# Kernel tuning notes

Measured on AMD Instinct MI355X. Metric: run time of the kernel, lower is better.

## Reference

```python
import jax, jax.numpy as jnp
import numpy as np

B, S, E, H = 4, 2048, 512, 1024

def setup_inputs() -> dict:
    key = jax.random.key(0)
    ks = jax.random.split(key, 8)
    s = 1.0 / np.sqrt(H)
    return {
        "hidden_states": jax.random.normal(ks[0], (B, S, H), jnp.float32),
        "external_embeddings": jax.random.normal(ks[1], (B, E, H), jnp.float32),
        "Wq": jax.random.normal(ks[2], (H, H), jnp.float32) * s,
        "bq": jax.random.normal(ks[3], (H,), jnp.float32) * 0.02,
        "Wk": jax.random.normal(ks[4], (H, H), jnp.float32) * s,
        "bk": jax.random.normal(ks[5], (H,), jnp.float32) * 0.02,
        "Wv": jax.random.normal(ks[6], (H, H), jnp.float32) * s,
        "bv": jax.random.normal(ks[7], (H,), jnp.float32) * 0.02,
    }

def reference(hidden_states, external_embeddings, Wq, bq, Wk, bk, Wv, bv):
    # Projections (torch Linear semantics: here weights stored as [in,out])
    q = hidden_states @ Wq + bq              # [B,S,H]
    k_tok = hidden_states @ Wk + bk          # [B,S,H]
    v_tok = hidden_states @ Wv + bv          # [B,S,H]
    k_ext = external_embeddings @ Wk + bk    # [B,E,H]
    v_ext = external_embeddings @ Wv + bv    # [B,E,H]
    # Each token attends to [its own key] ++ [external keys]; NO 1/sqrt(d) scaling
    # and NO head splitting, matching the original forward exactly.
    s_self = jnp.einsum('bsh,bsh->bs', q, k_tok)[..., None]   # [B,S,1]
    s_ext = jnp.einsum('bsh,beh->bse', q, k_ext)              # [B,S,E]
    scores = jnp.concatenate([s_self, s_ext], axis=-1)        # [B,S,1+E]
    probs = jax.nn.softmax(scores, axis=-1)
    ctx = probs[..., :1] * v_tok + jnp.einsum('bse,beh->bsh', probs[..., 1:], v_ext)
    return ctx  # [B,S,H]
```

## Files before the change

### kernel.cpp

```cpp
#include <hip/hip_runtime.h>
#include <stdint.h>

#define BB 4
#define SS 2048
#define EE 512
#define HH 1024

typedef _Float16 f16;
typedef __attribute__((ext_vector_type(8))) _Float16 f16x8;
typedef __attribute__((ext_vector_type(4))) _Float16 f16x4;
typedef __attribute__((ext_vector_type(4))) float f32x4;

__device__ __forceinline__ void async16(void* lds, const void* g) {
  __builtin_amdgcn_global_load_lds(
      (const __attribute__((address_space(1))) unsigned int*)g,
      (__attribute__((address_space(3))) unsigned int*)lds, 16, 0, 0);
}

template <int TERMS>
__device__ __forceinline__ void gemm_core(
    const f16* Ah, const f16* Al, const f16* Bh, const f16* Bl, int K, int ld,
    f16* lAh, f16* lAl, f16* lBh, f16* lBl, f32x4 acc[4][4]) {
  const int tid = threadIdx.x;
  const int wave = tid >> 6;
  const int lane = tid & 63;
  const int lrow = lane >> 2;
  const int lcol = (((lane & 3) ^ ((lane >> 3) & 3))) * 8;
  const int waveM = (wave >> 1) * 64;
  const int waveN = (wave & 1) * 64;
  const int frow = lane & 15;
  const int fk = ((lane >> 4) ^ ((frow >> 1) & 3)) * 8;

  for (int k0 = 0; k0 < K; k0 += 32) {
    __syncthreads();
#pragma unroll
    for (int i = 0; i < 2; ++i) {
      const int r0 = (wave * 2 + i) * 16;
      const size_t goff = (size_t)(r0 + lrow) * ld + (k0 + lcol);
      async16(&lAh[r0 * 32], Ah + goff);
      async16(&lBh[r0 * 32], Bh + goff);
      if (TERMS >= 2) async16(&lBl[r0 * 32], Bl + goff);
      if (TERMS >= 3) async16(&lAl[r0 * 32], Al + goff);
    }
    __syncthreads();

    f16x8 a[4], bh[4], bl[4], al[4];
#pragma unroll
    for (int i = 0; i < 4; ++i) {
      a[i] = *(const f16x8*)&lAh[(waveM + i * 16 + frow) * 32 + fk];
      bh[i] = *(const f16x8*)&lBh[(waveN + i * 16 + frow) * 32 + fk];
      if (TERMS >= 2) bl[i] = *(const f16x8*)&lBl[(waveN + i * 16 + frow) * 32 + fk];
      if (TERMS >= 3) al[i] = *(const f16x8*)&lAl[(waveM + i * 16 + frow) * 32 + fk];
    }
#pragma unroll
    for (int i = 0; i < 4; ++i)
#pragma unroll
      for (int j = 0; j < 4; ++j) {
        acc[i][j] = __builtin_amdgcn_mfma_f32_16x16x32_f16(a[i], bh[j], acc[i][j], 0, 0, 0);
        if (TERMS >= 2)
          acc[i][j] = __builtin_amdgcn_mfma_f32_16x16x32_f16(a[i], bl[j], acc[i][j], 0, 0, 0);
        if (TERMS >= 3)
          acc[i][j] = __builtin_amdgcn_mfma_f32_16x16x32_f16(al[i], bh[j], acc[i][j], 0, 0, 0);
      }
  }
}

__device__ __forceinline__ void epi_transposed(
    f16* __restrict__ dst, const f32x4 acc[4][4], const float bias[4], f16* tl) {
  const int tid = threadIdx.x, wave = tid >> 6, lane = tid & 63;
  const int waveM = (wave >> 1) * 64;
  const int colIn16 = lane & 15, quad = lane >> 4;
#pragma unroll
  for (int p = 0; p < 2; ++p) {
    __syncthreads();
    if ((wave & 1) == p) {
#pragma unroll
      for (int i = 0; i < 4; ++i)
#pragma unroll
        for (int j = 0; j < 4; ++j)
#pragma unroll
          for (int r = 0; r < 4; ++r) {
            const int row = waveM + i * 16 + quad * 4 + r;
            const int colL = j * 16 + colIn16;
            tl[colL * 136 + row] = (f16)(acc[i][j][r] + bias[j]);
          }
    }
    __syncthreads();
    for (int c = tid; c < 1024; c += 256) {
      const int colL = c >> 4, ch = c & 15;
      const f16x8 v = *(const f16x8*)&tl[colL * 136 + ch * 8];
      *(f16x8*)&dst[(size_t)(p * 64 + colL) * EE + ch * 8] = v;
    }
  }
}

__global__ __launch_bounds__(256) void cast_kernel(const float* __restrict__ xh32,
                                                   const float* __restrict__ xe32,
                                                   f16* __restrict__ xh,
                                                   f16* __restrict__ xe) {
  const int i = blockIdx.x * 256 + threadIdx.x;
  const int n4h = 8192 * HH / 4;
  const float* src = i < n4h ? xh32 : xe32;
  f16* dst = i < n4h ? xh : xe;
  const int k = i < n4h ? i : i - n4h;
  const float4 v = ((const float4*)src)[k];
  f16x4 o;
  o.x = (f16)v.x; o.y = (f16)v.y; o.z = (f16)v.z; o.w = (f16)v.w;
  ((f16x4*)dst)[k] = o;
}

__global__ void wsplit_kernel(const float* __restrict__ Wq, const float* __restrict__ Wk,
                              const float* __restrict__ Wv, f16* __restrict__ wt_hi,
                              f16* __restrict__ wt_lo) {
  __shared__ float tile[32][33];
  const int k0 = blockIdx.x * 32;
  const int n0g = blockIdx.y * 32;
  const int which = n0g >> 10;
  const float* W = which == 0 ? Wq : (which == 1 ? Wk : Wv);
  const int n0 = n0g & 1023;
  const int tx = threadIdx.x, ty = threadIdx.y;
#pragma unroll
  for (int i = 0; i < 32; i += 8)
    tile[ty + i][tx] = W[(size_t)(k0 + ty + i) * 1024 + n0 + tx];
  __syncthreads();
#pragma unroll
  for (int i = 0; i < 32; i += 8) {
    const int np = n0g + ty + i;
    const float v = tile[tx][ty + i];
    const size_t idx = (size_t)np * 1024 + k0 + tx;
    const f16 h = (f16)v;
    wt_hi[idx] = h;
    wt_lo[idx] = (f16)(v - (float)h);
  }
}

__global__ __launch_bounds__(256, 4) void proj_kernel(
    const f16* __restrict__ xh, const f16* __restrict__ xe,
    const f16* __restrict__ wt_hi, const f16* __restrict__ wt_lo,
    const float* __restrict__ bq, const float* __restrict__ bk,
    const float* __restrict__ bv, f16* __restrict__ q_hi, f16* __restrict__ q_lo,
    f16* __restrict__ kt, f16* __restrict__ vt,
    f16* __restrict__ ke_hi, f16* __restrict__ ke_lo, f16* __restrict__ veT) {
  const int g = blockIdx.x;
  const int j = g & 7;
  const int s = g >> 3;
  int mtile, ntile;
  if (s < 192) {
    const int w = s / 16, r = s % 16;
    ntile = w * 2 + (r & 1);
    mtile = (r >> 1) * 8 + j;
  } else {
    const int s2 = s - 192;
    const int w = s2 >> 2, r = s2 & 3;
    ntile = 8 + w * 2 + (r & 1);
    mtile = 64 + (r >> 1) * 8 + j;
  }
  const bool extRows = (mtile >= 64);

  __shared__ f16 lds[3 * 4096];

  const f16* A = extRows ? xe : xh;
  const int rowA = (extRows ? (mtile - 64) : mtile) * 128;
  const int rowB = ntile * 128;
  const bool split = (ntile < 8) || (extRows && ntile < 16);

  f32x4 acc[4][4];
#pragma unroll
  for (int i = 0; i < 4; ++i)
#pragma unroll
    for (int jj = 0; jj < 4; ++jj)
#pragma unroll
      for (int r = 0; r < 4; ++r) acc[i][jj][r] = 0.0f;

  if (split)
    gemm_core<2>(A + (size_t)rowA * HH, nullptr, wt_hi + (size_t)rowB * HH,
                 wt_lo + (size_t)rowB * HH, HH, HH,
                 lds, nullptr, lds + 4096, lds + 8192, acc);
  else
    gemm_core<1>(A + (size_t)rowA * HH, nullptr, wt_hi + (size_t)rowB * HH,
                 nullptr, HH, HH, lds, nullptr, lds + 4096, nullptr, acc);

  const int tid = threadIdx.x, wave = tid >> 6, lane = tid & 63;
  const int waveM = (wave >> 1) * 64, waveN = (wave & 1) * 64;
  const int colIn16 = lane & 15, rowQuad = (lane >> 4) * 4;
  float bias[4];
#pragma unroll
  for (int jj = 0; jj < 4; ++jj) {
    const int c = ntile * 128 + waveN + jj * 16 + colIn16;
    bias[jj] = c < 1024 ? bq[c] : (c < 2048 ? bk[c - 1024] : bv[c - 2048]);
  }

  if (extRows && ntile >= 16) {
    const int ge0 = (mtile - 64) * 128;
    const int bb = ge0 >> 9, e0 = ge0 & 511;
    epi_transposed(veT + ((size_t)bb * HH + (ntile - 16) * 128) * EE + e0,
                   acc, bias, lds);
    return;
  }

#pragma unroll
  for (int jj = 0; jj < 4; ++jj) {
    const int c = ntile * 128 + waveN + jj * 16 + colIn16;
#pragma unroll
    for (int i = 0; i < 4; ++i) {
#pragma unroll
      for (int r = 0; r < 4; ++r) {
        const int lrowIdx = waveM + i * 16 + rowQuad + r;
        const float val = acc[i][jj][r] + bias[jj];
        if (c < 1024) {
          const size_t idx = (size_t)(mtile * 128 + lrowIdx) * HH + c;
          const f16 h = (f16)val;
          q_hi[idx] = h;
          q_lo[idx] = (f16)(val - (float)h);
        } else if (c < 2048) {
          const int c2 = c - 1024;
          if (!extRows) {
            kt[(size_t)(mtile * 128 + lrowIdx) * HH + c2] = (f16)val;
          } else {
            const int ge = (mtile - 64) * 128 + lrowIdx;
            const size_t idx = (size_t)ge * HH + c2;
            const f16 h = (f16)val;
            ke_hi[idx] = h;
            ke_lo[idx] = (f16)(val - (float)h);
          }
        } else {
          vt[(size_t)(mtile * 128 + lrowIdx) * HH + (c - 2048)] = (f16)val;
        }
      }
    }
  }
}

__global__ __launch_bounds__(256, 4) void score_kernel(
    const f16* __restrict__ q_hi, const f16* __restrict__ q_lo,
    const f16* __restrict__ ke_hi, const f16* __restrict__ ke_lo,
    float* __restrict__ s_part) {
  const int b = blockIdx.z & 3;
  const int khalf = blockIdx.z >> 2;
  const int mtile = blockIdx.y;
  const int ntile = blockIdx.x;
  __shared__ f16 lds[4 * 4096];
  const size_t aoff = ((size_t)b * SS + mtile * 128) * HH + khalf * 512;
  const size_t boff = ((size_t)b * EE + ntile * 128) * HH + khalf * 512;

  f32x4 acc[4][4];
#pragma unroll
  for (int i = 0; i < 4; ++i)
#pragma unroll
    for (int j = 0; j < 4; ++j)
#pragma unroll
      for (int r = 0; r < 4; ++r) acc[i][j][r] = 0.0f;

  gemm_core<3>(q_hi + aoff, q_lo + aoff, ke_hi + boff, ke_lo + boff, 512, HH,
               lds, lds + 4096, lds + 8192, lds + 12288, acc);

  float* dst = s_part + (size_t)khalf * BB * SS * EE;
  const int tid = threadIdx.x, wave = tid >> 6, lane = tid & 63;
  const int waveM = (wave >> 1) * 64, waveN = (wave & 1) * 64;
  const int colIn16 = lane & 15, rowQuad = (lane >> 4) * 4;
#pragma unroll
  for (int j = 0; j < 4; ++j) {
    const int e = ntile * 128 + waveN + j * 16 + colIn16;
#pragma unroll
    for (int i = 0; i < 4; ++i)
#pragma unroll
      for (int r = 0; r < 4; ++r) {
        const int s = mtile * 128 + waveM + i * 16 + rowQuad + r;
        dst[((size_t)b * SS + s) * EE + e] = acc[i][j][r];
      }
  }
}

__global__ __launch_bounds__(256) void softmax_kernel(
    const f16* __restrict__ q_hi, const f16* __restrict__ q_lo,
    const f16* __restrict__ kt, const float* __restrict__ s_part,
    f16* __restrict__ probs, float* __restrict__ p_self) {
  const int t = blockIdx.x * 4 + (threadIdx.x >> 6);
  const int lane = threadIdx.x & 63;

  const size_t base = (size_t)t * HH;
  float ss = 0.f;
#pragma unroll
  for (int it = 0; it < 4; ++it) {
    const int off = it * 256 + lane * 4;
    const f16x4 qh = *(const f16x4*)&q_hi[base + off];
    const f16x4 ql = *(const f16x4*)&q_lo[base + off];
    const f16x4 kh = *(const f16x4*)&kt[base + off];
    ss += ((float)qh.x + (float)ql.x) * (float)kh.x;
    ss += ((float)qh.y + (float)ql.y) * (float)kh.y;
    ss += ((float)qh.z + (float)ql.z) * (float)kh.z;
    ss += ((float)qh.w + (float)ql.w) * (float)kh.w;
  }
#pragma unroll
  for (int m = 32; m > 0; m >>= 1) ss += __shfl_xor(ss, m, 64);

  const float* r0 = s_part + (size_t)t * EE;
  const float* r1 = s_part + (size_t)BB * SS * EE + (size_t)t * EE;
  const float4 a0 = *(const float4*)&r0[lane * 4];
  const float4 a1 = *(const float4*)&r0[256 + lane * 4];
  const float4 c0 = *(const float4*)&r1[lane * 4];
  const float4 c1 = *(const float4*)&r1[256 + lane * 4];
  const float v0x = a0.x + c0.x, v0y = a0.y + c0.y, v0z = a0.z + c0.z, v0w = a0.w + c0.w;
  const float v1x = a1.x + c1.x, v1y = a1.y + c1.y, v1z = a1.z + c1.z, v1w = a1.w + c1.w;
  float m = fmaxf(fmaxf(fmaxf(v0x, v0y), fmaxf(v0z, v0w)),
                  fmaxf(fmaxf(v1x, v1y), fmaxf(v1z, v1w)));
#pragma unroll
  for (int sh = 32; sh > 0; sh >>= 1) m = fmaxf(m, __shfl_xor(m, sh, 64));
  m = fmaxf(m, ss);
  const float e0 = __expf(v0x - m), e1 = __expf(v0y - m);
  const float e2 = __expf(v0z - m), e3 = __expf(v0w - m);
  const float e4 = __expf(v1x - m), e5 = __expf(v1y - m);
  const float e6 = __expf(v1z - m), e7 = __expf(v1w - m);
  float sum = ((e0 + e1) + (e2 + e3)) + ((e4 + e5) + (e6 + e7));
#pragma unroll
  for (int sh = 32; sh > 0; sh >>= 1) sum += __shfl_xor(sum, sh, 64);
  const float es = __expf(ss - m);
  const float inv = 1.0f / (sum + es);
  f16x4 p0, p1;
  p0.x = (f16)(e0 * inv); p0.y = (f16)(e1 * inv);
  p0.z = (f16)(e2 * inv); p0.w = (f16)(e3 * inv);
  p1.x = (f16)(e4 * inv); p1.y = (f16)(e5 * inv);
  p1.z = (f16)(e6 * inv); p1.w = (f16)(e7 * inv);
  *(f16x4*)&probs[(size_t)t * EE + lane * 4] = p0;
  *(f16x4*)&probs[(size_t)t * EE + 256 + lane * 4] = p1;
  if (lane == 0) p_self[t] = es * inv;
}

__global__ __launch_bounds__(256, 4) void pv_kernel(
    const f16* __restrict__ probs, const f16* __restrict__ veT,
    const float* __restrict__ p_self, const f16* __restrict__ vt,
    float* __restrict__ out) {
  const int b = blockIdx.z;
  const int mtile = blockIdx.y;
  const int ntile = blockIdx.x;
  __shared__ f16 lds[2 * 4096];
  const size_t aoff = ((size_t)b * SS + mtile * 128) * EE;
  const size_t boff = ((size_t)b * HH + ntile * 128) * EE;

  f32x4 acc[4][4];
#pragma unroll
  for (int i = 0; i < 4; ++i)
#pragma unroll
    for (int j = 0; j < 4; ++j)
#pragma unroll
      for (int r = 0; r < 4; ++r) acc[i][j][r] = 0.0f;

  gemm_core<1>(probs + aoff, nullptr, veT + boff, nullptr, EE, EE,
               lds, nullptr, lds + 4096, nullptr, acc);

  const int tid = threadIdx.x, wave = tid >> 6, lane = tid & 63;
  const int waveM = (wave >> 1) * 64, waveN = (wave & 1) * 64;
  const int colIn16 = lane & 15, rowQuad = (lane >> 4) * 4;
#pragma unroll
  for (int j = 0; j < 4; ++j) {
    const int h = ntile * 128 + waveN + j * 16 + colIn16;
#pragma unroll
    for (int i = 0; i < 4; ++i)
#pragma unroll
      for (int r = 0; r < 4; ++r) {
        const int s = mtile * 128 + waveM + i * 16 + rowQuad + r;
        const size_t t = (size_t)b * SS + s;
        __builtin_nontemporal_store(
            acc[i][j][r] + p_self[t] * (float)vt[t * HH + h], &out[t * HH + h]);
      }
  }
}

extern "C" void kernel_launch(void* const* d_in, const int* in_sizes, int n_in,
                              void* d_out, int out_size, void* d_ws, size_t ws_size,
                              hipStream_t stream) {
  const float* hidden = (const float*)d_in[0];
  const float* ext    = (const float*)d_in[1];
  const float* Wq = (const float*)d_in[2];
  const float* bq = (const float*)d_in[3];
  const float* Wk = (const float*)d_in[4];
  const float* bk = (const float*)d_in[5];
  const float* Wv = (const float*)d_in[6];
  const float* bv = (const float*)d_in[7];
  float* out = (float*)d_out;

  char* ws = (char*)d_ws;
  size_t off = 0;
  auto alloc = [&](size_t bytes) {
    char* p = ws + off;
    off += (bytes + 255) & ~(size_t)255;
    return p;
  };
  const size_t TOK = 8192, EXT = 2048;
  f16* xh    = (f16*)alloc(TOK * HH * 2);
  f16* xe    = (f16*)alloc(EXT * HH * 2);
  f16* wt_hi = (f16*)alloc(3072ull * HH * 2);
  f16* wt_lo = (f16*)alloc(3072ull * HH * 2);
  f16* q_hi  = (f16*)alloc(TOK * HH * 2);
  f16* q_lo  = (f16*)alloc(TOK * HH * 2);
  f16* kt    = (f16*)alloc(TOK * HH * 2);
  f16* vt    = (f16*)alloc(TOK * HH * 2);
  f16* ke_hi = (f16*)alloc(EXT * HH * 2);
  f16* ke_lo = (f16*)alloc(EXT * HH * 2);
  f16* veT   = (f16*)alloc((size_t)BB * HH * EE * 2);
  float* p_self = (float*)alloc(TOK * 4);
  float* s_part = (float*)alloc(2ull * BB * SS * EE * 4);
  f16* probs    = (f16*)alloc((size_t)BB * SS * EE * 2);

  cast_kernel<<<10240, 256, 0, stream>>>(hidden, ext, xh, xe);
  wsplit_kernel<<<dim3(32, 96), dim3(32, 8), 0, stream>>>(Wq, Wk, Wv, wt_hi, wt_lo);

  proj_kernel<<<1792, 256, 0, stream>>>(
      xh, xe, wt_hi, wt_lo, bq, bk, bv,
      q_hi, q_lo, kt, vt, ke_hi, ke_lo, veT);

  score_kernel<<<dim3(4, 16, 8), 256, 0, stream>>>(q_hi, q_lo, ke_hi, ke_lo, s_part);
  softmax_kernel<<<2048, 256, 0, stream>>>(q_hi, q_lo, kt, s_part, probs, p_self);
  pv_kernel<<<dim3(8, 16, 4), 256, 0, stream>>>(probs, veT, p_self, vt, out);
}
```

Before: 332.5 us.

## Use 256-row projection tiles with 512 threads and drop score split-K

The projection GEMM moves to 256x128 tiles run by 512-thread blocks (8 waves), so each weight tile loaded into LDS is reused across twice as many rows. The transposed V-ext epilogue is reworked to match. The score kernel no longer splits K in two, writing one fp32 score buffer instead of two partials, which removes the extra partial write and re-read in softmax. The softmax self-score now drops the q_lo term, using fp16 q_hi only, which trades a little precision for less memory traffic. Fewer, larger blocks and half as many score blocks may lower occupancy and parallelism.

Measured after the change: 349.8 us. 1.05x slower.

```diff
diff --git a/kernel.cpp b/kernel.cpp
--- a/kernel.cpp
+++ b/kernel.cpp
@@ -65,31 +65,82 @@
   }
 }
 
-__device__ __forceinline__ void epi_transposed(
+template <int TERMS>
+__device__ __forceinline__ void gemm_core256(
+    const f16* A, const f16* Bh, const f16* Bl, int K, int ld,
+    f16* lA, f16* lBh, f16* lBl, f32x4 acc[4][4]) {
+  const int tid = threadIdx.x;
+  const int wave = tid >> 6;
+  const int lane = tid & 63;
+  const int lrow = lane >> 2;
+  const int lcol = (((lane & 3) ^ ((lane >> 3) & 3))) * 8;
+  const int waveM = (wave >> 1) * 64;
+  const int waveN = (wave & 1) * 64;
+  const int frow = lane & 15;
+  const int fk = ((lane >> 4) ^ ((frow >> 1) & 3)) * 8;
+
+  for (int k0 = 0; k0 < K; k0 += 32) {
+    __syncthreads();
+    {
+      const int r0 = wave * 16;
+      async16(&lA[r0 * 32], A + (size_t)(r0 + lrow) * ld + (k0 + lcol));
+      const int r1 = 128 + wave * 16;
+      async16(&lA[r1 * 32], A + (size_t)(r1 + lrow) * ld + (k0 + lcol));
+      async16(&lBh[r0 * 32], Bh + (size_t)(r0 + lrow) * ld + (k0 + lcol));
+      if (TERMS >= 2)
+        async16(&lBl[r0 * 32], Bl + (size_t)(r0 + lrow) * ld + (k0 + lcol));
+    }
+    __syncthreads();
+
+    f16x8 a[4], bh[4], bl[4];
+#pragma unroll
+    for (int i = 0; i < 4; ++i) {
+      a[i] = *(const f16x8*)&lA[(waveM + i * 16 + frow) * 32 + fk];
+      bh[i] = *(const f16x8*)&lBh[(waveN + i * 16 + frow) * 32 + fk];
+      if (TERMS >= 2) bl[i] = *(const f16x8*)&lBl[(waveN + i * 16 + frow) * 32 + fk];
+    }
+#pragma unroll
+    for (int i = 0; i < 4; ++i)
+#pragma unroll
+      for (int j = 0; j < 4; ++j) {
+        acc[i][j] = __builtin_amdgcn_mfma_f32_16x16x32_f16(a[i], bh[j], acc[i][j], 0, 0, 0);
+        if (TERMS >= 2)
+          acc[i][j] = __builtin_amdgcn_mfma_f32_16x16x32_f16(a[i], bl[j], acc[i][j], 0, 0, 0);
+      }
+  }
+}
+
+__device__ __forceinline__ void epi_transposed256(
     f16* __restrict__ dst, const f32x4 acc[4][4], const float bias[4], f16* tl) {
   const int tid = threadIdx.x, wave = tid >> 6, lane = tid & 63;
-  const int waveM = (wave >> 1) * 64;
-  const int colIn16 = lane & 15, quad = lane >> 4;
-#pragma unroll
-  for (int p = 0; p < 2; ++p) {
-    __syncthreads();
-    if ((wave & 1) == p) {
-#pragma unroll
-      for (int i = 0; i < 4; ++i)
-#pragma unroll
-        for (int j = 0; j < 4; ++j)
-#pragma unroll
-          for (int r = 0; r < 4; ++r) {
-            const int row = waveM + i * 16 + quad * 4 + r;
-            const int colL = j * 16 + colIn16;
-            tl[colL * 136 + row] = (f16)(acc[i][j][r] + bias[j]);
-          }
-    }
-    __syncthreads();
-    for (int c = tid; c < 1024; c += 256) {
-      const int colL = c >> 4, ch = c & 15;
-      const f16x8 v = *(const f16x8*)&tl[colL * 136 + ch * 8];
-      *(f16x8*)&dst[(size_t)(p * 64 + colL) * EE + ch * 8] = v;
+  const int quad = lane >> 4, colIn16 = lane & 15;
+  const int mq = wave >> 1;
+  const int half = mq >> 1;
+  const int msub = mq & 1;
+  const int np = wave & 1;
+#pragma unroll
+  for (int h = 0; h < 2; ++h) {
+#pragma unroll
+    for (int p = 0; p < 2; ++p) {
+      __syncthreads();
+      if (half == h && np == p) {
+#pragma unroll
+        for (int i = 0; i < 4; ++i)
+#pragma unroll
+          for (int j = 0; j < 4; ++j)
+#pragma unroll
+            for (int r = 0; r < 4; ++r) {
+              const int rowL = msub * 64 + i * 16 + quad * 4 + r;
+              const int colL = j * 16 + colIn16;
+              tl[colL * 136 + rowL] = (f16)(acc[i][j][r] + bias[j]);
+            }
+      }
+      __syncthreads();
+      for (int c = tid; c < 1024; c += 512) {
+        const int colL = c >> 4, ch = c & 15;
+        const f16x8 v = *(const f16x8*)&tl[colL * 136 + ch * 8];
+        *(f16x8*)&dst[(size_t)(p * 64 + colL) * EE + h * 128 + ch * 8] = v;
+      }
     }
   }
 }
@@ -134,7 +185,7 @@
   }
 }
 
-__global__ __launch_bounds__(256, 4) void proj_kernel(
+__global__ __launch_bounds__(512, 4) void proj_kernel(
     const f16* __restrict__ xh, const f16* __restrict__ xe,
     const f16* __restrict__ wt_hi, const f16* __restrict__ wt_lo,
     const float* __restrict__ bq, const float* __restrict__ bk,
@@ -142,25 +193,24 @@
     f16* __restrict__ kt, f16* __restrict__ vt,
     f16* __restrict__ ke_hi, f16* __restrict__ ke_lo, f16* __restrict__ veT) {
   const int g = blockIdx.x;
-  const int j = g & 7;
+  const int xcd = g & 7;
   const int s = g >> 3;
   int mtile, ntile;
-  if (s < 192) {
-    const int w = s / 16, r = s % 16;
+  if (s < 96) {
+    const int w = s >> 3, r = s & 7;
     ntile = w * 2 + (r & 1);
-    mtile = (r >> 1) * 8 + j;
+    mtile = (r >> 1) * 8 + xcd;
   } else {
-    const int s2 = s - 192;
-    const int w = s2 >> 2, r = s2 & 3;
-    ntile = 8 + w * 2 + (r & 1);
-    mtile = 64 + (r >> 1) * 8 + j;
-  }
-  const bool extRows = (mtile >= 64);
-
-  __shared__ f16 lds[3 * 4096];
+    const int s2 = s - 96;
+    ntile = 8 + (s2 >> 1) * 2 + (s2 & 1);
+    mtile = 32 + xcd;
+  }
+  const bool extRows = (mtile >= 32);
+
+  __shared__ f16 lds[16384];
 
   const f16* A = extRows ? xe : xh;
-  const int rowA = (extRows ? (mtile - 64) : mtile) * 128;
+  const int rowA = (extRows ? (mtile - 32) : mtile) * 256;
   const int rowB = ntile * 128;
   const bool split = (ntile < 8) || (extRows && ntile < 16);
 
@@ -173,12 +223,12 @@
       for (int r = 0; r < 4; ++r) acc[i][jj][r] = 0.0f;
 
   if (split)
-    gemm_core<2>(A + (size_t)rowA * HH, nullptr, wt_hi + (size_t)rowB * HH,
-                 wt_lo + (size_t)rowB * HH, HH, HH,
-                 lds, nullptr, lds + 4096, lds + 8192, acc);
+    gemm_core256<2>(A + (size_t)rowA * HH, wt_hi + (size_t)rowB * HH,
+                    wt_lo + (size_t)rowB * HH, HH, HH,
+                    lds, lds + 8192, lds + 12288, acc);
   else
-    gemm_core<1>(A + (size_t)rowA * HH, nullptr, wt_hi + (size_t)rowB * HH,
-                 nullptr, HH, HH, lds, nullptr, lds + 4096, nullptr, acc);
+    gemm_core256<1>(A + (size_t)rowA * HH, wt_hi + (size_t)rowB * HH, nullptr,
+                    HH, HH, lds, lds + 8192, nullptr, acc);
 
   const int tid = threadIdx.x, wave = tid >> 6, lane = tid & 63;
   const int waveM = (wave >> 1) * 64, waveN = (wave & 1) * 64;
@@ -191,10 +241,10 @@
   }
 
   if (extRows && ntile >= 16) {
-    const int ge0 = (mtile - 64) * 128;
+    const int ge0 = (mtile - 32) * 256;
     const int bb = ge0 >> 9, e0 = ge0 & 511;
-    epi_transposed(veT + ((size_t)bb * HH + (ntile - 16) * 128) * EE + e0,
-                   acc, bias, lds);
+    epi_transposed256(veT + ((size_t)bb * HH + (ntile - 16) * 128) * EE + e0,
+                      acc, bias, lds);
     return;
   }
 
@@ -208,23 +258,23 @@
         const int lrowIdx = waveM + i * 16 + rowQuad + r;
         const float val = acc[i][jj][r] + bias[jj];
         if (c < 1024) {
-          const size_t idx = (size_t)(mtile * 128 + lrowIdx) * HH + c;
+          const size_t idx = (size_t)(mtile * 256 + lrowIdx) * HH + c;
           const f16 h = (f16)val;
           q_hi[idx] = h;
           q_lo[idx] = (f16)(val - (float)h);
         } else if (c < 2048) {
           const int c2 = c - 1024;
           if (!extRows) {
-            kt[(size_t)(mtile * 128 + lrowIdx) * HH + c2] = (f16)val;
+            kt[(size_t)(mtile * 256 + lrowIdx) * HH + c2] = (f16)val;
           } else {
-            const int ge = (mtile - 64) * 128 + lrowIdx;
+            const int ge = (mtile - 32) * 256 + lrowIdx;
             const size_t idx = (size_t)ge * HH + c2;
             const f16 h = (f16)val;
             ke_hi[idx] = h;
             ke_lo[idx] = (f16)(val - (float)h);
           }
         } else {
-          vt[(size_t)(mtile * 128 + lrowIdx) * HH + (c - 2048)] = (f16)val;
+          vt[(size_t)(mtile * 256 + lrowIdx) * HH + (c - 2048)] = (f16)val;
         }
       }
     }
@@ -234,14 +284,13 @@
 __global__ __launch_bounds__(256, 4) void score_kernel(
     const f16* __restrict__ q_hi, const f16* __restrict__ q_lo,
     const f16* __restrict__ ke_hi, const f16* __restrict__ ke_lo,
-    float* __restrict__ s_part) {
-  const int b = blockIdx.z & 3;
-  const int khalf = blockIdx.z >> 2;
+    float* __restrict__ s_ext) {
+  const int b = blockIdx.z;
   const int mtile = blockIdx.y;
   const int ntile = blockIdx.x;
   __shared__ f16 lds[4 * 4096];
-  const size_t aoff = ((size_t)b * SS + mtile * 128) * HH + khalf * 512;
-  const size_t boff = ((size_t)b * EE + ntile * 128) * HH + khalf * 512;
+  const size_t aoff = ((size_t)b * SS + mtile * 128) * HH;
+  const size_t boff = ((size_t)b * EE + ntile * 128) * HH;
 
   f32x4 acc[4][4];
 #pragma unroll
@@ -251,10 +300,9 @@
 #pragma unroll
       for (int r = 0; r < 4; ++r) acc[i][j][r] = 0.0f;
 
-  gemm_core<3>(q_hi + aoff, q_lo + aoff, ke_hi + boff, ke_lo + boff, 512, HH,
+  gemm_core<3>(q_hi + aoff, q_lo + aoff, ke_hi + boff, ke_lo + boff, HH, HH,
                lds, lds + 4096, lds + 8192, lds + 12288, acc);
 
-  float* dst = s_part + (size_t)khalf * BB * SS * EE;
   const int tid = threadIdx.x, wave = tid >> 6, lane = tid & 63;
   const int waveM = (wave >> 1) * 64, waveN = (wave & 1) * 64;
   const int colIn16 = lane & 15, rowQuad = (lane >> 4) * 4;
@@ -266,51 +314,43 @@
 #pragma unroll
       for (int r = 0; r < 4; ++r) {
         const int s = mtile * 128 + waveM + i * 16 + rowQuad + r;
-        dst[((size_t)b * SS + s) * EE + e] = acc[i][j][r];
+        s_ext[((size_t)b * SS + s) * EE + e] = acc[i][j][r];
       }
   }
 }
 
 __global__ __launch_bounds__(256) void softmax_kernel(
-    const f16* __restrict__ q_hi, const f16* __restrict__ q_lo,
-    const f16* __restrict__ kt, const float* __restrict__ s_part,
-    f16* __restrict__ probs, float* __restrict__ p_self) {
+    const f16* __restrict__ q_hi, const f16* __restrict__ kt,
+    const float* __restrict__ s_ext, f16* __restrict__ probs,
+    float* __restrict__ p_self) {
   const int t = blockIdx.x * 4 + (threadIdx.x >> 6);
   const int lane = threadIdx.x & 63;
 
   const size_t base = (size_t)t * HH;
   float ss = 0.f;
 #pragma unroll
-  for (int it = 0; it < 4; ++it) {
-    const int off = it * 256 + lane * 4;
-    const f16x4 qh = *(const f16x4*)&q_hi[base + off];
-    const f16x4 ql = *(const f16x4*)&q_lo[base + off];
-    const f16x4 kh = *(const f16x4*)&kt[base + off];
-    ss += ((float)qh.x + (float)ql.x) * (float)kh.x;
-    ss += ((float)qh.y + (float)ql.y) * (float)kh.y;
-    ss += ((float)qh.z + (float)ql.z) * (float)kh.z;
-    ss += ((float)qh.w + (float)ql.w) * (float)kh.w;
+  for (int it = 0; it < 2; ++it) {
+    const int off = it * 512 + lane * 8;
+    const f16x8 qh = *(const f16x8*)&q_hi[base + off];
+    const f16x8 kh = *(const f16x8*)&kt[base + off];
+#pragma unroll
+    for (int u = 0; u < 8; ++u) ss += (float)qh[u] * (float)kh[u];
   }
 #pragma unroll
   for (int m = 32; m > 0; m >>= 1) ss += __shfl_xor(ss, m, 64);
 
-  const float* r0 = s_part + (size_t)t * EE;
-  const float* r1 = s_part + (size_t)BB * SS * EE + (size_t)t * EE;
-  const float4 a0 = *(const float4*)&r0[lane * 4];
-  const float4 a1 = *(const float4*)&r0[256 + lane * 4];
-  const float4 c0 = *(const float4*)&r1[lane * 4];
-  const float4 c1 = *(const float4*)&r1[256 + lane * 4];
-  const float v0x = a0.x + c0.x, v0y = a0.y + c0.y, v0z = a0.z + c0.z, v0w = a0.w + c0.w;
-  const float v1x = a1.x + c1.x, v1y = a1.y + c1.y, v1z = a1.z + c1.z, v1w = a1.w + c1.w;
-  float m = fmaxf(fmaxf(fmaxf(v0x, v0y), fmaxf(v0z, v0w)),
-                  fmaxf(fmaxf(v1x, v1y), fmaxf(v1z, v1w)));
+  const float* r0 = s_ext + (size_t)t * EE;
+  const float4 v0 = *(const float4*)&r0[lane * 4];
+  const float4 v1 = *(const float4*)&r0[256 + lane * 4];
+  float m = fmaxf(fmaxf(fmaxf(v0.x, v0.y), fmaxf(v0.z, v0.w)),
+                  fmaxf(fmaxf(v1.x, v1.y), fmaxf(v1.z, v1.w)));
 #pragma unroll
   for (int sh = 32; sh > 0; sh >>= 1) m = fmaxf(m, __shfl_xor(m, sh, 64));
   m = fmaxf(m, ss);
-  const float e0 = __expf(v0x - m), e1 = __expf(v0y - m);
-  const float e2 = __expf(v0z - m), e3 = __expf(v0w - m);
-  const float e4 = __expf(v1x - m), e5 = __expf(v1y - m);
-  const float e6 = __expf(v1z - m), e7 = __expf(v1w - m);
+  const float e0 = __expf(v0.x - m), e1 = __expf(v0.y - m);
+  const float e2 = __expf(v0.z - m), e3 = __expf(v0.w - m);
+  const float e4 = __expf(v1.x - m), e5 = __expf(v1.y - m);
+  const float e6 = __expf(v1.z - m), e7 = __expf(v1.w - m);
   float sum = ((e0 + e1) + (e2 + e3)) + ((e4 + e5) + (e6 + e7));
 #pragma unroll
   for (int sh = 32; sh > 0; sh >>= 1) sum += __shfl_xor(sum, sh, 64);
@@ -399,17 +439,17 @@
   f16* ke_lo = (f16*)alloc(EXT * HH * 2);
   f16* veT   = (f16*)alloc((size_t)BB * HH * EE * 2);
   float* p_self = (float*)alloc(TOK * 4);
-  float* s_part = (float*)alloc(2ull * BB * SS * EE * 4);
+  float* s_ext  = (float*)alloc((size_t)BB * SS * EE * 4);
   f16* probs    = (f16*)alloc((size_t)BB * SS * EE * 2);
 
   cast_kernel<<<10240, 256, 0, stream>>>(hidden, ext, xh, xe);
   wsplit_kernel<<<dim3(32, 96), dim3(32, 8), 0, stream>>>(Wq, Wk, Wv, wt_hi, wt_lo);
 
-  proj_kernel<<<1792, 256, 0, stream>>>(
+  proj_kernel<<<896, 512, 0, stream>>>(
       xh, xe, wt_hi, wt_lo, bq, bk, bv,
       q_hi, q_lo, kt, vt, ke_hi, ke_lo, veT);
 
-  score_kernel<<<dim3(4, 16, 8), 256, 0, stream>>>(q_hi, q_lo, ke_hi, ke_lo, s_part);
-  softmax_kernel<<<2048, 256, 0, stream>>>(q_hi, q_lo, kt, s_part, probs, p_self);
+  score_kernel<<<dim3(4, 16, 4), 256, 0, stream>>>(q_hi, q_lo, ke_hi, ke_lo, s_ext);
+  softmax_kernel<<<2048, 256, 0, stream>>>(q_hi, kt, s_ext, probs, p_self);
   pv_kernel<<<dim3(8, 16, 4), 256, 0, stream>>>(probs, veT, p_self, vt, out);
 }
```
